# Performance work log

Hardware: AMD Instinct MI355X
Metric: run time of the kernel (lower is better)

## Reference

```python
import jax, jax.numpy as jnp
import numpy as np

B, D, S = 4096, 1024, 1024

def setup_inputs() -> dict:
    key = jax.random.key(0)
    ks = jax.random.split(key, 12)
    u = lambda k, shp: jax.random.uniform(k, shp, jnp.float32, -0.05, 0.05)
    return {
        "inputs": jax.random.normal(ks[0], (B, D), jnp.float32),
        "h0": jax.random.normal(ks[1], (B, S), jnp.float32),
        "c0": jax.random.normal(ks[2], (B, S), jnp.float32),
        "w_f": u(ks[3], (D, S)), "u_f": u(ks[4], (S, S)), "b_f": u(ks[5], (S,)),
        "w_i": u(ks[6], (D, S)), "u_i": u(ks[7], (S, S)), "b_i": u(ks[8], (S,)),
        "w_o": u(ks[9], (D, S)), "u_o": u(ks[10], (S, S)), "b_o": u(ks[11], (S,)),
    }

def reference(inputs, h0, c0, w_f, u_f, b_f, w_i, u_i, b_i, w_o, u_o, b_o):
    # Faithful to the original: input_cell reuses the FORGET gate weights and
    # sigmoid (not tanh, not w_c) -- a quirk of the source module.
    pre_f = inputs @ w_f + h0 @ u_f + b_f          # [B, S]
    forget_gate = jax.nn.sigmoid(pre_f)
    input_gate = jax.nn.sigmoid(inputs @ w_i + h0 @ u_i + b_i)
    output_gate = jax.nn.sigmoid(inputs @ w_o + h0 @ u_o + b_o)
    input_cell = jax.nn.sigmoid(pre_f)             # same pre-activation as forget gate
    c_new = forget_gate * c0 + input_cell * input_gate
    h_new = output_gate * jnp.tanh(c_new)
    return (h_new, c_new)
```

## Files before the change

kernel.cpp:

```cpp
#include <hip/hip_runtime.h>
#include <cstdint>
#include <cstddef>


typedef __attribute__((ext_vector_type(8))) short bf16x8;
typedef __attribute__((ext_vector_type(4))) float f32x4;
typedef __attribute__((ext_vector_type(8))) short s16x8;
typedef __attribute__((ext_vector_type(4))) float f32x4v;

#define MROWS 4096
#define KDIM  1024
#define NCOLS 1024

__device__ __forceinline__ short f2bf(float f) {
    uint32_t u = __builtin_bit_cast(uint32_t, f);
    u += 0x7fffu + ((u >> 16) & 1u);
    return (short)(u >> 16);
}

__global__ void cvt_bf16_kernel(const float* __restrict__ x,
                                const float* __restrict__ h,
                                short* __restrict__ xb,
                                short* __restrict__ hb) {
    int b = blockIdx.x;
    const float* in;
    short* out;
    if (b < 2048) { in = x; out = xb; }
    else          { in = h; out = hb; b -= 2048; }
    const int i = (b * 256 + threadIdx.x) * 8;
    f32x4v a = *(const f32x4v*)(in + i);
    f32x4v c = *(const f32x4v*)(in + i + 4);
    s16x8 o;
    o[0] = f2bf(a[0]); o[1] = f2bf(a[1]); o[2] = f2bf(a[2]); o[3] = f2bf(a[3]);
    o[4] = f2bf(c[0]); o[5] = f2bf(c[1]); o[6] = f2bf(c[2]); o[7] = f2bf(c[3]);
    *(s16x8*)(out + i) = o;
}

struct W6 {
    const float* src[6];
    short* dst[6];
};

__global__ void transpose_cvt_kernel(W6 p) {
    __shared__ short tile[32][33];
    const float* __restrict__ w  = p.src[blockIdx.z];
    short* __restrict__       wt = p.dst[blockIdx.z];
    const int tx = threadIdx.x & 31;
    const int ty = threadIdx.x >> 5;
    const int kbase = blockIdx.y * 32;
    const int nbase = blockIdx.x * 32;
#pragma unroll
    for (int r = 0; r < 4; ++r) {
        int k = kbase + ty + r * 8;
        tile[ty + r * 8][tx] = f2bf(w[k * NCOLS + nbase + tx]);
    }
    __syncthreads();
#pragma unroll
    for (int r = 0; r < 4; ++r) {
        int n = nbase + ty + r * 8;
        wt[n * KDIM + kbase + tx] = tile[tx][ty + r * 8];
    }
}

__global__ __launch_bounds__(512)
void lstm_gemm_kernel(const short* __restrict__ Xb, const short* __restrict__ Hb,
                      const short* __restrict__ WT0, const short* __restrict__ WT1,
                      const short* __restrict__ WT2,
                      const short* __restrict__ UT0, const short* __restrict__ UT1,
                      const short* __restrict__ UT2,
                      const float* __restrict__ bf_, const float* __restrict__ bi_,
                      const float* __restrict__ bo_,
                      const float* __restrict__ c0,
                      float* __restrict__ outH, float* __restrict__ outC) {
    __shared__ __align__(16) short lds[2][16384];

    const int tid  = threadIdx.x;
    const int lane = tid & 63;
    const int wave = tid >> 6;
    const int wm   = wave >> 2;
    const int wn   = wave & 3;
    const int m0   = blockIdx.y * 128;
    const int n0   = blockIdx.x * 128;

    const int l15 = lane & 15;
    const int q   = lane >> 4;

    f32x4 acc[3][4][2] = {};

    const int srow   = tid >> 2;
    const int schunk = (tid & 3) ^ ((tid >> 3) & 3);
    const int skoff  = schunk * 8;

    int aOff[4], bOff[2];
#pragma unroll
    for (int m = 0; m < 4; ++m) {
        const int row = wm * 64 + m * 16 + l15;
        aOff[m] = row * 64 + ((q ^ ((row >> 1) & 3)) << 4);
    }
#pragma unroll
    for (int n = 0; n < 2; ++n) {
        const int row = wn * 32 + n * 16 + l15;
        bOff[n] = row * 64 + ((q ^ ((row >> 1) & 3)) << 4);
    }

    auto stage = [&](int buf, int kt) {
        const bool second = kt >= 32;
        const short* aS = second ? Hb  : Xb;
        const short* s0 = second ? UT0 : WT0;
        const short* s1 = second ? UT1 : WT1;
        const short* s2 = second ? UT2 : WT2;
        const int kk = (kt & 31) * 32 + skoff;
#pragma unroll
        for (int r = 0; r < 4; ++r) {
            const short* src = (r == 0) ? aS : (r == 1 ? s0 : (r == 2 ? s1 : s2));
            const int rbase = (r == 0) ? m0 : n0;
            const char* g = (const char*)(src + (size_t)(rbase + srow) * KDIM + kk);
            __builtin_amdgcn_global_load_lds(
                (const __attribute__((address_space(1))) unsigned int*)(uintptr_t)g,
                (__attribute__((address_space(3))) unsigned int*)(uintptr_t)
                    ((char*)&lds[buf][0] + r * 8192 + tid * 16),
                16, 0, 0);
        }
    };

    stage(0, 0);
    __syncthreads();

    int buf = 0;
    for (int kt = 0; kt < 64; ++kt) {
        if (kt < 63) stage(buf ^ 1, kt + 1);

        const char* L = (const char*)&lds[buf][0];
        bf16x8 af[4];
#pragma unroll
        for (int m = 0; m < 4; ++m)
            af[m] = *(const bf16x8*)(L + aOff[m]);
#pragma unroll
        for (int g3 = 0; g3 < 3; ++g3) {
#pragma unroll
            for (int n = 0; n < 2; ++n) {
                bf16x8 bv = *(const bf16x8*)(L + 8192 * (1 + g3) + bOff[n]);
#pragma unroll
                for (int m = 0; m < 4; ++m)
                    acc[g3][m][n] = __builtin_amdgcn_mfma_f32_16x16x32_bf16(
                        af[m], bv, acc[g3][m][n], 0, 0, 0);
            }
        }
        __syncthreads();
        buf ^= 1;
    }

    const int rj = (lane >> 4) * 4;
#pragma unroll
    for (int m = 0; m < 4; ++m) {
#pragma unroll
        for (int n = 0; n < 2; ++n) {
            const int col = n0 + wn * 32 + n * 16 + l15;
            const float bfv = bf_[col], biv = bi_[col], bov = bo_[col];
            const f32x4 pf = acc[0][m][n];
            const f32x4 pi = acc[1][m][n];
            const f32x4 po = acc[2][m][n];
#pragma unroll
            for (int j = 0; j < 4; ++j) {
                const int row = m0 + wm * 64 + m * 16 + rj + j;
                const float fg = 1.f / (1.f + __expf(-(pf[j] + bfv)));
                const float ig = 1.f / (1.f + __expf(-(pi[j] + biv)));
                const float og = 1.f / (1.f + __expf(-(po[j] + bov)));
                const float cv = c0[row * NCOLS + col];
                const float cn = fg * cv + fg * ig;
                const float e  = __expf(-2.f * cn);
                const float th = (1.f - e) / (1.f + e);
                outH[row * NCOLS + col] = og * th;
                outC[row * NCOLS + col] = cn;
            }
        }
    }
}

extern "C" void kernel_launch(void* const* d_in, const int* in_sizes, int n_in,
                              void* d_out, int out_size, void* d_ws, size_t ws_size,
                              hipStream_t stream) {
    const float* inputs = (const float*)d_in[0];
    const float* h0     = (const float*)d_in[1];
    const float* c0     = (const float*)d_in[2];
    const float* w_f    = (const float*)d_in[3];
    const float* u_f    = (const float*)d_in[4];
    const float* b_f    = (const float*)d_in[5];
    const float* w_i    = (const float*)d_in[6];
    const float* u_i    = (const float*)d_in[7];
    const float* b_i    = (const float*)d_in[8];
    const float* w_o    = (const float*)d_in[9];
    const float* u_o    = (const float*)d_in[10];
    const float* b_o    = (const float*)d_in[11];

    float* outH = (float*)d_out;
    float* outC = outH + (size_t)MROWS * NCOLS;

    char* ws = (char*)d_ws;
    short* Xb  = (short*)(ws);
    short* Hb  = (short*)(ws + (8u << 20));
    short* WT0 = (short*)(ws + (16u << 20));
    short* WT1 = (short*)(ws + (18u << 20));
    short* WT2 = (short*)(ws + (20u << 20));
    short* UT0 = (short*)(ws + (22u << 20));
    short* UT1 = (short*)(ws + (24u << 20));
    short* UT2 = (short*)(ws + (26u << 20));

    cvt_bf16_kernel<<<4096, 256, 0, stream>>>(inputs, h0, Xb, Hb);

    W6 p;
    p.src[0] = w_f; p.src[1] = w_i; p.src[2] = w_o;
    p.src[3] = u_f; p.src[4] = u_i; p.src[5] = u_o;
    p.dst[0] = WT0; p.dst[1] = WT1; p.dst[2] = WT2;
    p.dst[3] = UT0; p.dst[4] = UT1; p.dst[5] = UT2;
    transpose_cvt_kernel<<<dim3(32, 32, 6), 256, 0, stream>>>(p);

    dim3 grid(NCOLS / 128, MROWS / 128);
    lstm_gemm_kernel<<<grid, 512, 0, stream>>>(
        Xb, Hb, WT0, WT1, WT2, UT0, UT1, UT2,
        b_f, b_i, b_o, c0, outH, outC);
}
```

Before: 84.71 us.

## Deepen GEMM LDS pipeline to four buffers with explicit vmcnt waits

Changes the fused LSTM GEMM from a double-buffered loop to a four-buffer ring that prefetches two k-tiles ahead. Each step waits with explicit s_waitcnt vmcnt counts and a single raw s_barrier instead of __syncthreads. All B fragments are loaded before the MFMA block, and the MFMA section runs at raised wave priority. The aim is to hide global-to-LDS load latency and cut barrier stalls. The cost is doubling LDS to 128KB per block, which lowers occupancy, and the correctness of the hand-counted vmcnt values depends on how the compiler emits the loads.

After: 77.23 us. 8.8% less time.

```diff
diff --git a/kernel.cpp b/kernel.cpp
--- a/kernel.cpp
+++ b/kernel.cpp
@@ -72,7 +72,7 @@
                       const float* __restrict__ bo_,
                       const float* __restrict__ c0,
                       float* __restrict__ outH, float* __restrict__ outC) {
-    __shared__ __align__(16) short lds[2][16384];
+    __shared__ __align__(16) short lds[4][16384];
 
     const int tid  = threadIdx.x;
     const int lane = tid & 63;
@@ -123,32 +123,48 @@
         }
     };
 
-    stage(0, 0);
-    __syncthreads();
-
-    int buf = 0;
-    for (int kt = 0; kt < 64; ++kt) {
-        if (kt < 63) stage(buf ^ 1, kt + 1);
-
+    auto compute = [&](int buf) {
         const char* L = (const char*)&lds[buf][0];
         bf16x8 af[4];
 #pragma unroll
         for (int m = 0; m < 4; ++m)
             af[m] = *(const bf16x8*)(L + aOff[m]);
-#pragma unroll
-        for (int g3 = 0; g3 < 3; ++g3) {
-#pragma unroll
-            for (int n = 0; n < 2; ++n) {
-                bf16x8 bv = *(const bf16x8*)(L + 8192 * (1 + g3) + bOff[n]);
+        bf16x8 bv[3][2];
+#pragma unroll
+        for (int g3 = 0; g3 < 3; ++g3)
+#pragma unroll
+            for (int n = 0; n < 2; ++n)
+                bv[g3][n] = *(const bf16x8*)(L + 8192 * (1 + g3) + bOff[n]);
+        __builtin_amdgcn_s_setprio(1);
+#pragma unroll
+        for (int g3 = 0; g3 < 3; ++g3)
+#pragma unroll
+            for (int n = 0; n < 2; ++n)
 #pragma unroll
                 for (int m = 0; m < 4; ++m)
                     acc[g3][m][n] = __builtin_amdgcn_mfma_f32_16x16x32_bf16(
-                        af[m], bv, acc[g3][m][n], 0, 0, 0);
-            }
-        }
-        __syncthreads();
-        buf ^= 1;
-    }
+                        af[m], bv[g3][n], acc[g3][m][n], 0, 0, 0);
+        __builtin_amdgcn_s_setprio(0);
+    };
+
+    stage(0, 0);
+    stage(1, 1);
+
+    for (int kt = 0; kt < 62; ++kt) {
+        stage((kt + 2) & 3, kt + 2);
+        asm volatile("s_waitcnt vmcnt(8)" ::: "memory");
+        __builtin_amdgcn_s_barrier();
+        __builtin_amdgcn_sched_barrier(0);
+        compute(kt & 3);
+    }
+    asm volatile("s_waitcnt vmcnt(4)" ::: "memory");
+    __builtin_amdgcn_s_barrier();
+    __builtin_amdgcn_sched_barrier(0);
+    compute(62 & 3);
+    asm volatile("s_waitcnt vmcnt(0)" ::: "memory");
+    __builtin_amdgcn_s_barrier();
+    __builtin_amdgcn_sched_barrier(0);
+    compute(63 & 3);
 
     const int rj = (lane >> 4) * 4;
 #pragma unroll
```

## Deepen GEMM pipeline with 4-stage LDS ring and register double-buffered fragments

Applied to the files above, without the earlier changes.

Replaces the 2-buffer LDS loop in the fused LSTM GEMM with a 4-deep ring of asynchronous global-to-LDS stages, paced by explicit vmcnt waits and raw barriers. LDS fragment reads for the next k-step are double-buffered in registers so they can overlap the current MFMA block, and that block is wrapped in s_setprio. The aim is to hide global-load and LDS latency behind matrix math. In exchange, LDS use doubles, and the launch_bounds(512,2) hint tightens the register budget. With the accumulators plus two fragment sets this may force spills.

Result: faster. 76.98 us (-9.1%).

```diff
diff --git a/kernel.cpp b/kernel.cpp
--- a/kernel.cpp
+++ b/kernel.cpp
@@ -62,7 +62,7 @@
     }
 }
 
-__global__ __launch_bounds__(512)
+__global__ __launch_bounds__(512, 2)
 void lstm_gemm_kernel(const short* __restrict__ Xb, const short* __restrict__ Hb,
                       const short* __restrict__ WT0, const short* __restrict__ WT1,
                       const short* __restrict__ WT2,
@@ -72,7 +72,7 @@
                       const float* __restrict__ bo_,
                       const float* __restrict__ c0,
                       float* __restrict__ outH, float* __restrict__ outC) {
-    __shared__ __align__(16) short lds[2][16384];
+    __shared__ __align__(16) short lds[4][16384];
 
     const int tid  = threadIdx.x;
     const int lane = tid & 63;
@@ -123,32 +123,90 @@
         }
     };
 
+    bf16x8 fa0[4], fb0[6], fa1[4], fb1[6];
+
+#define READF(FA, FB, BUF)                                                   \
+    {                                                                        \
+        const char* L_ = (const char*)&lds[(BUF)][0];                        \
+        _Pragma("unroll")                                                    \
+        for (int m_ = 0; m_ < 4; ++m_)                                       \
+            FA[m_] = *(const bf16x8*)(L_ + aOff[m_]);                        \
+        _Pragma("unroll")                                                    \
+        for (int g_ = 0; g_ < 3; ++g_)                                       \
+            _Pragma("unroll")                                                \
+            for (int n_ = 0; n_ < 2; ++n_)                                   \
+                FB[g_ * 2 + n_] =                                            \
+                    *(const bf16x8*)(L_ + 8192 * (1 + g_) + bOff[n_]);       \
+    }
+
+#define MFMAC(FA, FB)                                                        \
+    {                                                                        \
+        __builtin_amdgcn_s_setprio(1);                                       \
+        _Pragma("unroll")                                                    \
+        for (int g_ = 0; g_ < 3; ++g_)                                       \
+            _Pragma("unroll")                                                \
+            for (int n_ = 0; n_ < 2; ++n_)                                   \
+                _Pragma("unroll")                                            \
+                for (int m_ = 0; m_ < 4; ++m_)                               \
+                    acc[g_][m_][n_] = __builtin_amdgcn_mfma_f32_16x16x32_bf16(\
+                        FA[m_], FB[g_ * 2 + n_], acc[g_][m_][n_], 0, 0, 0);  \
+        __builtin_amdgcn_s_setprio(0);                                       \
+    }
+
+#define WAITV(N) asm volatile("s_waitcnt vmcnt(" #N ")" ::: "memory")
+#define WAITL0   asm volatile("s_waitcnt lgkmcnt(0)" ::: "memory")
+#define BAR      __builtin_amdgcn_s_barrier()
+#define SCHED0   __builtin_amdgcn_sched_barrier(0)
+
     stage(0, 0);
-    __syncthreads();
-
-    int buf = 0;
-    for (int kt = 0; kt < 64; ++kt) {
-        if (kt < 63) stage(buf ^ 1, kt + 1);
-
-        const char* L = (const char*)&lds[buf][0];
-        bf16x8 af[4];
-#pragma unroll
-        for (int m = 0; m < 4; ++m)
-            af[m] = *(const bf16x8*)(L + aOff[m]);
-#pragma unroll
-        for (int g3 = 0; g3 < 3; ++g3) {
-#pragma unroll
-            for (int n = 0; n < 2; ++n) {
-                bf16x8 bv = *(const bf16x8*)(L + 8192 * (1 + g3) + bOff[n]);
-#pragma unroll
-                for (int m = 0; m < 4; ++m)
-                    acc[g3][m][n] = __builtin_amdgcn_mfma_f32_16x16x32_bf16(
-                        af[m], bv, acc[g3][m][n], 0, 0, 0);
-            }
-        }
-        __syncthreads();
-        buf ^= 1;
-    }
+    stage(1, 1);
+    stage(2, 2);
+    WAITV(8);
+    BAR;
+    SCHED0;
+    READF(fa0, fb0, 0);
+    WAITL0;
+
+    for (int kt = 0; kt < 60; kt += 2) {
+        stage((kt + 3) & 3, kt + 3);
+        WAITV(8);
+        BAR;
+        SCHED0;
+        READF(fa1, fb1, (kt + 1) & 3);
+        MFMAC(fa0, fb0);
+        WAITL0;
+        stage((kt + 4) & 3, kt + 4);
+        WAITV(8);
+        BAR;
+        SCHED0;
+        READF(fa0, fb0, (kt + 2) & 3);
+        MFMAC(fa1, fb1);
+        WAITL0;
+    }
+
+    stage(63 & 3, 63);
+    WAITV(8);
+    BAR;
+    SCHED0;
+    READF(fa1, fb1, 61 & 3);
+    MFMAC(fa0, fb0);
+    WAITL0;
+
+    WAITV(4);
+    BAR;
+    SCHED0;
+    READF(fa0, fb0, 62 & 3);
+    MFMAC(fa1, fb1);
+    WAITL0;
+
+    WAITV(0);
+    BAR;
+    SCHED0;
+    READF(fa1, fb1, 63 & 3);
+    MFMAC(fa0, fb0);
+    WAITL0;
+
+    MFMAC(fa1, fb1);
 
     const int rj = (lane >> 4) * 4;
 #pragma unroll
@@ -175,6 +233,12 @@
             }
         }
     }
+#undef READF
+#undef MFMAC
+#undef WAITV
+#undef WAITL0
+#undef BAR
+#undef SCHED0
 }
 
 extern "C" void kernel_launch(void* const* d_in, const int* in_sizes, int n_in,
```

## Deepen GEMM pipeline to four LDS stages with interleaved loads and MFMA

Applied to the files above, without the earlier changes.

Replaces the double-buffered main loop with a four-buffer ring that prefetches three k-tiles ahead and uses explicit vmcnt waits. Global-to-LDS stage loads are split and interleaved between the per-gate MFMA groups, with sched barriers and setprio to keep the matrix cores busy. It also requests two blocks per CU through launch bounds. LDS use per block doubles to 128 KB, which may prevent two blocks from co-residing, and the extra barriers add synchronisation overhead.

Result: faster. 79.45 us (-6.2%).

```diff
diff --git a/kernel.cpp b/kernel.cpp
--- a/kernel.cpp
+++ b/kernel.cpp
@@ -62,7 +62,7 @@
     }
 }
 
-__global__ __launch_bounds__(512)
+__global__ __launch_bounds__(512, 2)
 void lstm_gemm_kernel(const short* __restrict__ Xb, const short* __restrict__ Hb,
                       const short* __restrict__ WT0, const short* __restrict__ WT1,
                       const short* __restrict__ WT2,
@@ -72,7 +72,7 @@
                       const float* __restrict__ bo_,
                       const float* __restrict__ c0,
                       float* __restrict__ outH, float* __restrict__ outC) {
-    __shared__ __align__(16) short lds[2][16384];
+    __shared__ __align__(16) short lds[4][16384];
 
     const int tid  = threadIdx.x;
     const int lane = tid & 63;
@@ -87,9 +87,8 @@
 
     f32x4 acc[3][4][2] = {};
 
-    const int srow   = tid >> 2;
-    const int schunk = (tid & 3) ^ ((tid >> 3) & 3);
-    const int skoff  = schunk * 8;
+    const int srow  = tid >> 2;
+    const int skoff = ((tid & 3) ^ ((tid >> 3) & 3)) * 8;
 
     int aOff[4], bOff[2];
 #pragma unroll
@@ -103,52 +102,96 @@
         bOff[n] = row * 64 + ((q ^ ((row >> 1) & 3)) << 4);
     }
 
-    auto stage = [&](int buf, int kt) {
+    auto stageR = [&](int buf, int kt, int r) {
         const bool second = kt >= 32;
-        const short* aS = second ? Hb  : Xb;
-        const short* s0 = second ? UT0 : WT0;
-        const short* s1 = second ? UT1 : WT1;
-        const short* s2 = second ? UT2 : WT2;
-        const int kk = (kt & 31) * 32 + skoff;
-#pragma unroll
-        for (int r = 0; r < 4; ++r) {
-            const short* src = (r == 0) ? aS : (r == 1 ? s0 : (r == 2 ? s1 : s2));
-            const int rbase = (r == 0) ? m0 : n0;
-            const char* g = (const char*)(src + (size_t)(rbase + srow) * KDIM + kk);
-            __builtin_amdgcn_global_load_lds(
-                (const __attribute__((address_space(1))) unsigned int*)(uintptr_t)g,
-                (__attribute__((address_space(3))) unsigned int*)(uintptr_t)
-                    ((char*)&lds[buf][0] + r * 8192 + tid * 16),
-                16, 0, 0);
-        }
+        const short* src;
+        int rbase;
+        if (r == 0)      { src = second ? Hb  : Xb;  rbase = m0; }
+        else if (r == 1) { src = second ? UT0 : WT0; rbase = n0; }
+        else if (r == 2) { src = second ? UT1 : WT1; rbase = n0; }
+        else             { src = second ? UT2 : WT2; rbase = n0; }
+        const char* g = (const char*)(src + (size_t)(rbase + srow) * KDIM +
+                                      (kt & 31) * 32 + skoff);
+        __builtin_amdgcn_global_load_lds(
+            (const __attribute__((address_space(1))) unsigned int*)(uintptr_t)g,
+            (__attribute__((address_space(3))) unsigned int*)(uintptr_t)
+                ((char*)&lds[buf][0] + r * 8192 + tid * 16),
+            16, 0, 0);
     };
 
-    stage(0, 0);
-    __syncthreads();
-
-    int buf = 0;
-    for (int kt = 0; kt < 64; ++kt) {
-        if (kt < 63) stage(buf ^ 1, kt + 1);
-
-        const char* L = (const char*)&lds[buf][0];
-        bf16x8 af[4];
-#pragma unroll
-        for (int m = 0; m < 4; ++m)
-            af[m] = *(const bf16x8*)(L + aOff[m]);
-#pragma unroll
-        for (int g3 = 0; g3 < 3; ++g3) {
-#pragma unroll
-            for (int n = 0; n < 2; ++n) {
-                bf16x8 bv = *(const bf16x8*)(L + 8192 * (1 + g3) + bOff[n]);
-#pragma unroll
-                for (int m = 0; m < 4; ++m)
-                    acc[g3][m][n] = __builtin_amdgcn_mfma_f32_16x16x32_bf16(
-                        af[m], bv, acc[g3][m][n], 0, 0, 0);
-            }
-        }
-        __syncthreads();
-        buf ^= 1;
-    }
+#define WAITL0   asm volatile("s_waitcnt lgkmcnt(0)" ::: "memory")
+#define BAR      __builtin_amdgcn_s_barrier()
+#define SCHED0   __builtin_amdgcn_sched_barrier(0)
+
+#define MFMA8(G, AF, BV0, BV1)                                               \
+    {                                                                        \
+        __builtin_amdgcn_s_setprio(1);                                       \
+        _Pragma("unroll")                                                    \
+        for (int m_ = 0; m_ < 4; ++m_)                                       \
+            acc[G][m_][0] = __builtin_amdgcn_mfma_f32_16x16x32_bf16(         \
+                AF[m_], BV0, acc[G][m_][0], 0, 0, 0);                        \
+        _Pragma("unroll")                                                    \
+        for (int m_ = 0; m_ < 4; ++m_)                                       \
+            acc[G][m_][1] = __builtin_amdgcn_mfma_f32_16x16x32_bf16(         \
+                AF[m_], BV1, acc[G][m_][1], 0, 0, 0);                        \
+        __builtin_amdgcn_s_setprio(0);                                       \
+    }
+
+#define STEP(WVTOK, KT, DOSTAGE)                                             \
+    {                                                                        \
+        const int kt_ = (KT);                                                \
+        const char* L_ = (const char*)&lds[kt_ & 3][0];                      \
+        asm volatile("s_waitcnt vmcnt(" WVTOK ")" ::: "memory");             \
+        BAR;                           \
+        SCHED0;                                                              \
+                \
+        bf16x8 af[4], bv0a, bv0b, bv1a, bv1b, bv2a, bv2b;                    \
+        _Pragma("unroll")                                                    \
+        for (int m_ = 0; m_ < 4; ++m_)                                       \
+            af[m_] = *(const bf16x8*)(L_ + aOff[m_]);                        \
+        bv0a = *(const bf16x8*)(L_ + 8192 + bOff[0]);                        \
+        bv0b = *(const bf16x8*)(L_ + 8192 + bOff[1]);                        \
+        if (DOSTAGE) { stageR((kt_ + 3) & 3, kt_ + 3, 0);                    \
+                       stageR((kt_ + 3) & 3, kt_ + 3, 1); }                  \
+        BAR;                                                                 \
+        WAITL0;                                                              \
+        SCHED0;                                                              \
+        MFMA8(0, af, bv0a, bv0b);                                            \
+        BAR;                                                                 \
+        SCHED0;                                                              \
+                    \
+        bv1a = *(const bf16x8*)(L_ + 16384 + bOff[0]);                       \
+        bv1b = *(const bf16x8*)(L_ + 16384 + bOff[1]);                       \
+        if (DOSTAGE) { stageR((kt_ + 3) & 3, kt_ + 3, 2);                    \
+                       stageR((kt_ + 3) & 3, kt_ + 3, 3); }                  \
+        BAR;                                                                 \
+        WAITL0;                                                              \
+        SCHED0;                                                              \
+        MFMA8(1, af, bv1a, bv1b);                                            \
+        BAR;                                                                 \
+        SCHED0;                                                              \
+                               \
+        bv2a = *(const bf16x8*)(L_ + 24576 + bOff[0]);                       \
+        bv2b = *(const bf16x8*)(L_ + 24576 + bOff[1]);                       \
+        BAR;                                                                 \
+        WAITL0;                                                              \
+        SCHED0;                                                              \
+        MFMA8(2, af, bv2a, bv2b);                                            \
+    }
+
+#pragma unroll
+    for (int r = 0; r < 4; ++r) stageR(0, 0, r);
+#pragma unroll
+    for (int r = 0; r < 4; ++r) stageR(1, 1, r);
+#pragma unroll
+    for (int r = 0; r < 4; ++r) stageR(2, 2, r);
+
+    for (int kt = 0; kt <= 60; ++kt) {
+        STEP("8", kt, true);
+    }
+    STEP("8", 61, false);
+    STEP("4", 62, false);
+    STEP("0", 63, false);
 
     const int rj = (lane >> 4) * 4;
 #pragma unroll
@@ -175,6 +218,11 @@
             }
         }
     }
+#undef STEP
+#undef MFMA8
+#undef WAITL0
+#undef BAR
+#undef SCHED0
 }
 
 extern "C" void kernel_launch(void* const* d_in, const int* in_sizes, int n_in,
```
